# Optimization experiments

Hardware: AMD Instinct MI355X
Metric: run time of the kernel (lower is better)

## Reference

```python
import jax, jax.numpy as jnp
import numpy as np
from jax import lax

B, S, F, H, C = 256, 14, 1024, 1024, 2513


def setup_inputs() -> dict:
    key = jax.random.key(0)
    ks = jax.random.split(key, 12)
    s = 1.0 / np.sqrt(H)  # PyTorch LSTM/Linear init range
    u = lambda k, shape: jax.random.uniform(k, shape, jnp.float32, -s, s)
    return {
        "inputs": jax.random.normal(ks[0], (B, S, F), jnp.float32),
        # rolling LSTM params (PyTorch gate order: i, f, g, o)
        "Wih_r": u(ks[1], (4 * H, F)), "Whh_r": u(ks[2], (4 * H, H)),
        "bih_r": u(ks[3], (4 * H,)), "bhh_r": u(ks[4], (4 * H,)),
        # unrolling LSTM params
        "Wih_u": u(ks[5], (4 * H, F)), "Whh_u": u(ks[6], (4 * H, H)),
        "bih_u": u(ks[7], (4 * H,)), "bhh_u": u(ks[8], (4 * H,)),
        # classifier
        "Wc": u(ks[9], (C, H)), "bc": u(ks[10], (C,)),
    }


def _gate_update(gates, c):
    i, f, g, o = jnp.split(gates, 4, axis=-1)
    c2 = jax.nn.sigmoid(f) * c + jax.nn.sigmoid(i) * jnp.tanh(g)
    h2 = jax.nn.sigmoid(o) * jnp.tanh(c2)
    return h2, c2


def reference(inputs, Wih_r, Whh_r, bih_r, bhh_r, Wih_u, Whh_u, bih_u, bhh_u, Wc, bc):
    # dropout layers are identity (eval mode)
    x = inputs.transpose(1, 0, 2)  # [S, B, F]

    # --- rolling LSTM: collect h, c at every timestep ---
    xg_r = jnp.einsum('sbf,gf->sbg', x, Wih_r) + bih_r + bhh_r  # [S,B,4H]

    def roll_step(carry, xg_t):
        h, c = carry
        h2, c2 = _gate_update(xg_t + h @ Whh_r.T, c)
        return (h2, c2), (h2, c2)

    z = jnp.zeros((B, H), inputs.dtype)
    _, (hs, cs) = lax.scan(roll_step, (z, z), xg_r)  # [S,B,H] each

    # --- unrolling LSTM: for each t, feed inputs[t] repeated (S - t + 1) times,
    # starting from (hs[t], cs[t]); keep the final hidden state.
    # Vectorized: run S+1 steps for every t, gather step index S-t.
    xg_u = jnp.einsum('sbf,gf->sbg', x, Wih_u) + bih_u + bhh_u  # [S,B,4H] (input constant per t)

    def unroll_one(xg_t, h0, c0):
        def step(carry, _):
            h, c = carry
            h2, c2 = _gate_update(xg_t + h @ Whh_u.T, c)
            return (h2, c2), h2
        _, hs_all = lax.scan(step, (h0, c0), None, length=S + 1)
        return hs_all  # [S+1, B, H]

    allh = jax.vmap(unroll_one)(xg_u, hs, cs)  # [S, S+1, B, H]
    t_idx = jnp.arange(S)
    h_n = allh[t_idx, S - t_idx]  # last hidden of each length-(S-t+1) unroll -> [S,B,H]

    preds = h_n.transpose(1, 0, 2)  # [B, S, H]
    y = preds @ Wc.T + bc  # [B, S, C]
    return y
```

## Files before the change

### kernel.cpp

```cpp
#include <hip/hip_runtime.h>
#include <hip/hip_bf16.h>

#define GLOBAL_AS __attribute__((address_space(1)))
#define LDS_AS    __attribute__((address_space(3)))

typedef __bf16 bf16_t;
typedef __bf16 bf16x8 __attribute__((ext_vector_type(8)));
typedef __bf16 bf16x4 __attribute__((ext_vector_type(4)));
typedef float  f32x4  __attribute__((ext_vector_type(4)));
typedef _Float16 fp16_t;
typedef _Float16 fp16x8 __attribute__((ext_vector_type(8)));

static constexpr int Bb = 256;
static constexpr int Ss = 14;
static constexpr int Hh = 1024;
static constexpr int Cc = 2513;
static constexpr int NXc = 3584;
static constexpr int Kk = 1024;

__device__ __forceinline__ float sigm(float x)   { return 1.0f / (1.0f + __expf(-x)); }
__device__ __forceinline__ float tanh_f(float x) { return 2.0f / (1.0f + __expf(-2.0f * x)) - 1.0f; }

template<int EPI>
__global__ __launch_bounds__(256, 2)
void gemm_bt(const bf16_t* __restrict__ A, const bf16_t* __restrict__ Bm,
             int N, int rpg, int cpg, int CG, int CB,
             const float* __restrict__ e_bias,
             bf16_t* __restrict__ xg_bf,
             float* __restrict__ fout)
{
    const int lin = blockIdx.x;
    const int xcd = lin & 7;
    const int per = lin >> 3;
    const int rg = xcd / CG, cg = xcd % CG;
    const int rb = rg * rpg + per % rpg;
    const int cb = cg * cpg + per / rpg;
    if (cb >= CB) return;

    __shared__ char smem[32768];
    LDS_AS char* sA = (LDS_AS char*)smem;
    LDS_AS char* sB = sA + 16384;

    const int tid  = threadIdx.x;
    const int lane = tid & 63;
    const int wave = tid >> 6;
    const int row0 = rb * 128;
    const int col0 = cb * 128;
    const int mwb  = (wave >> 1) * 64;
    const int nwb  = (wave & 1) * 64;
    const int quad = lane >> 4;
    const int l15  = lane & 15;

    f32x4 acc[4][4] = {};

    for (int kb = 0; kb < Kk; kb += 64) {
#pragma unroll
        for (int it = 0; it < 4; ++it) {
            int c  = it * 256 + tid;
            int m  = c >> 3;
            int kq = (c & 7) ^ (m & 7);
            size_t arow;
            if (EPI == 2) {
                int row = row0 + m;
                int bb = row / 14;
                int ss = row - bb * 14;
                arow = (size_t)(ss * 256 + bb);
            } else {
                arow = (size_t)(row0 + m);
            }
            const bf16_t* ga = A + arow * Kk + kb + kq * 8;
            int nr = col0 + m;
            if (EPI == 2) { if (nr >= N) nr = 0; }
            const bf16_t* gb = Bm + (size_t)nr * Kk + kb + kq * 8;
            LDS_AS char* la = sA + (size_t)(it * 256 + (tid & 192)) * 16;
            LDS_AS char* lb = sB + (size_t)(it * 256 + (tid & 192)) * 16;
            __builtin_amdgcn_global_load_lds((const GLOBAL_AS void*)ga, (LDS_AS void*)la, 16, 0, 0);
            __builtin_amdgcn_global_load_lds((const GLOBAL_AS void*)gb, (LDS_AS void*)lb, 16, 0, 0);
        }
        __syncthreads();

#pragma unroll
        for (int kt = 0; kt < 2; ++kt) {
            bf16x8 af[4], bfr[4];
            const int kq = kt * 4 + quad;
#pragma unroll
            for (int i = 0; i < 4; ++i) {
                int ml = mwb + i * 16 + l15;
                af[i]  = *(const LDS_AS bf16x8*)(sA + (size_t)(ml * 8 + (kq ^ (ml & 7))) * 16);
                int nl = nwb + i * 16 + l15;
                bfr[i] = *(const LDS_AS bf16x8*)(sB + (size_t)(nl * 8 + (kq ^ (nl & 7))) * 16);
            }
#pragma unroll
            for (int i = 0; i < 4; ++i)
#pragma unroll
                for (int j = 0; j < 4; ++j)
                    acc[i][j] = __builtin_amdgcn_mfma_f32_16x16x32_bf16(af[i], bfr[j], acc[i][j], 0, 0, 0);
        }
        __syncthreads();
    }

#pragma unroll
    for (int im = 0; im < 4; ++im) {
#pragma unroll
        for (int jn = 0; jn < 4; ++jn) {
            const int rr  = row0 + mwb + im * 16 + quad * 4;
            const int col = col0 + nwb + jn * 16 + l15;
            f32x4 v = acc[im][jn];
            if (EPI == 0) {
                const int n = rr >> 2;
                f32x4 bi = *(const f32x4*)(e_bias + n * 4);
                bf16x4 o;
                o[0] = (bf16_t)(v[0] + bi[0]); o[1] = (bf16_t)(v[1] + bi[1]);
                o[2] = (bf16_t)(v[2] + bi[2]); o[3] = (bf16_t)(v[3] + bi[3]);
                *(bf16x4*)(xg_bf + ((size_t)n * NXc + col) * 4) = o;
            } else {
                if (col < N) {
                    float bi = e_bias[col];
#pragma unroll
                    for (int g = 0; g < 4; ++g)
                        fout[(size_t)(rr + g) * N + col] = v[g] + bi;
                }
            }
        }
    }
}

struct StepArgs {
    const bf16_t* Au;
    const bf16_t* Ar;
    const bf16_t* Bh;
    const bf16_t* xg_u;
    const bf16_t* xg_r;
    const fp16_t* c_r;
    fp16_t*       c_w;
    bf16_t*       h_w;
    const bf16_t* Wih;
    const bf16_t* Xb;
    const float*  bias2;
    bf16_t*       XG2;
    int UCB;
    int b_off;
    int xg_off;
    int cr_off;
    int cw_off;
    int CB, cpg;
    int nRec;
    int xp[7];
};

__global__ __launch_bounds__(256, 2)
void lstm_step(StepArgs p)
{
    const int tid  = threadIdx.x;
    const int lane = tid & 63;
    const int wave = tid >> 6;
    const int mwb  = (wave >> 1) * 64;
    const int nwb  = (wave & 1) * 64;
    const int quad = lane >> 4;
    const int l15  = lane & 15;

    __shared__ char smem[32768];
    LDS_AS char* sA = (LDS_AS char*)smem;
    LDS_AS char* sB = sA + 16384;

    const bf16_t* A;
    const bf16_t* Bbase;
    int row0, bcol0;
    bool isxp;
    bool roll = false;
    int  colb = 0;

    if ((int)blockIdx.x >= p.nRec) {
        isxp = true;
        const int idx = (int)blockIdx.x - p.nRec;
        const int c   = p.xp[idx >> 6];
        const int isu = (c >= 14) ? 1 : 0;
        const int j   = c - isu * 14;
        const int rb  = idx & 31;
        const int cbl = (idx >> 5) & 1;
        row0  = isu * 4096 + rb * 128;
        bcol0 = j * 256 + cbl * 128;
        A     = p.Wih;
        Bbase = p.Xb;
    } else {
        isxp = false;
        const int lin = blockIdx.x;
        const int xcd = lin & 7;
        const int per = lin >> 3;
        const int rb = (xcd >> 2) * 16 + (per & 15);
        const int cb = (xcd & 3) * p.cpg + (per >> 4);
        if (cb >= p.CB) return;
        roll = (cb >= p.UCB);
        colb = roll ? (cb - p.UCB) : cb;
        A     = roll ? p.Ar : p.Au;
        Bbase = p.Bh;
        row0  = rb * 128;
        bcol0 = colb * 128 + (roll ? p.b_off : 0);
    }

    f32x4 acc[4][4] = {};

    for (int kb = 0; kb < Kk; kb += 64) {
#pragma unroll
        for (int it = 0; it < 4; ++it) {
            int c  = it * 256 + tid;
            int m  = c >> 3;
            int kq = (c & 7) ^ (m & 7);
            const bf16_t* ga = A     + (size_t)(row0  + m) * Kk + kb + kq * 8;
            const bf16_t* gb = Bbase + (size_t)(bcol0 + m) * Kk + kb + kq * 8;
            LDS_AS char* la = sA + (size_t)(it * 256 + (tid & 192)) * 16;
            LDS_AS char* lb = sB + (size_t)(it * 256 + (tid & 192)) * 16;
            __builtin_amdgcn_global_load_lds((const GLOBAL_AS void*)ga, (LDS_AS void*)la, 16, 0, 0);
            __builtin_amdgcn_global_load_lds((const GLOBAL_AS void*)gb, (LDS_AS void*)lb, 16, 0, 0);
        }
        __syncthreads();

#pragma unroll
        for (int kt = 0; kt < 2; ++kt) {
            bf16x8 af[4], bfr[4];
            const int kq = kt * 4 + quad;
#pragma unroll
            for (int i = 0; i < 4; ++i) {
                int ml = mwb + i * 16 + l15;
                af[i]  = *(const LDS_AS bf16x8*)(sA + (size_t)(ml * 8 + (kq ^ (ml & 7))) * 16);
                int nl = nwb + i * 16 + l15;
                bfr[i] = *(const LDS_AS bf16x8*)(sB + (size_t)(nl * 8 + (kq ^ (nl & 7))) * 16);
            }
#pragma unroll
            for (int i = 0; i < 4; ++i)
#pragma unroll
                for (int j = 0; j < 4; ++j)
                    acc[i][j] = __builtin_amdgcn_mfma_f32_16x16x32_bf16(af[i], bfr[j], acc[i][j], 0, 0, 0);
        }
        __syncthreads();
    }

    if (isxp) {
#pragma unroll
        for (int im = 0; im < 4; ++im) {
#pragma unroll
            for (int jn = 0; jn < 4; ++jn) {
                const int rr  = row0 + mwb + im * 16 + quad * 4;
                const int col = bcol0 + nwb + jn * 16 + l15;
                f32x4 v = acc[im][jn];
                const int n = rr >> 2;
                f32x4 bi = *(const f32x4*)(p.bias2 + n * 4);
                bf16x4 o;
                o[0] = (bf16_t)(v[0] + bi[0]); o[1] = (bf16_t)(v[1] + bi[1]);
                o[2] = (bf16_t)(v[2] + bi[2]); o[3] = (bf16_t)(v[3] + bi[3]);
                *(bf16x4*)(p.XG2 + ((size_t)n * NXc + col) * 4) = o;
            }
        }
        return;
    }

    const bf16_t* xg = roll ? p.xg_r : p.xg_u;
    const int xo  = roll ? p.xg_off : 0;
    const int cro = roll ? p.cr_off : 0;
    const int cwo = roll ? p.cw_off : 0;
    const int nbase = row0 >> 2;

#pragma unroll
    for (int im = 0; im < 4; ++im)
#pragma unroll
        for (int jn = 0; jn < 4; ++jn) {
            const int rr  = row0 + mwb + im * 16 + quad * 4;
            const int col = colb * 128 + nwb + jn * 16 + l15;
            const int n = rr >> 2;
            bf16x4 xg4 = *(const bf16x4*)(xg + ((size_t)n * NXc + (col + xo)) * 4);
            acc[im][jn][0] += (float)xg4[0];
            acc[im][jn][1] += (float)xg4[1];
            acc[im][jn][2] += (float)xg4[2];
            acc[im][jn][3] += (float)xg4[3];
        }

    LDS_AS f32x4* sG = (LDS_AS f32x4*)smem;

#pragma unroll
    for (int pass = 0; pass < 2; ++pass) {
        if ((wave & 1) == pass) {
            const int nw = (wave >> 1) * 16;
#pragma unroll
            for (int im = 0; im < 4; ++im)
#pragma unroll
                for (int jn = 0; jn < 4; ++jn) {
                    const int n_l = nw + im * 4 + quad;
                    const int c_l = jn * 16 + l15;
                    sG[c_l * 32 + (n_l ^ (c_l & 7))] = acc[im][jn];
                }
        }
        __syncthreads();
        {
            const int c_l  = tid >> 2;
            const int nb   = (tid & 3) * 8;
            const int colg = colb * 128 + pass * 64 + c_l;
            const fp16_t* crp = p.c_r + (size_t)(colg + cro) * Hh + nbase + nb;
            fp16x8 c8 = *(const fp16x8*)crp;
            bf16x8 h8o; fp16x8 c8o;
#pragma unroll
            for (int j = 0; j < 8; ++j) {
                f32x4 g = sG[c_l * 32 + ((nb + j) ^ (c_l & 7))];
                float c2 = sigm(g[1]) * (float)c8[j] + sigm(g[0]) * tanh_f(g[2]);
                float h2 = sigm(g[3]) * tanh_f(c2);
                c8o[j] = (fp16_t)c2;
                h8o[j] = (bf16_t)h2;
            }
            *(fp16x8*)(p.c_w + (size_t)(colg + cwo) * Hh + nbase + nb) = c8o;
            *(bf16x8*)(p.h_w + (size_t)(colg + cwo) * Hh + nbase + nb) = h8o;
        }
        if (pass == 0) __syncthreads();
    }
}

__global__ void cvt_w(const float* __restrict__ a0, const float* __restrict__ a1,
                      const float* __restrict__ a2, const float* __restrict__ a3,
                      bf16_t* __restrict__ o0, bf16_t* __restrict__ o1,
                      bf16_t* __restrict__ o2, bf16_t* __restrict__ o3)
{
    int idx = blockIdx.x * 256 + threadIdx.x;
    int mat = idx >> 20;
    int r   = (idx >> 8) & 4095;
    int k4  = (idx & 255) * 4;
    int n = r >> 2, g = r & 3;
    const float* src = mat == 0 ? a0 : mat == 1 ? a1 : mat == 2 ? a2 : a3;
    bf16_t*      dst = mat == 0 ? o0 : mat == 1 ? o1 : mat == 2 ? o2 : o3;
    f32x4 v = *(const f32x4*)(src + (size_t)(g * Hh + n) * Kk + k4);
    bf16x4 o;
    o[0] = (bf16_t)v[0]; o[1] = (bf16_t)v[1]; o[2] = (bf16_t)v[2]; o[3] = (bf16_t)v[3];
    *(bf16x4*)(dst + (size_t)r * Kk + k4) = o;
}

__global__ void cvt_bias(const float* __restrict__ bih_r, const float* __restrict__ bhh_r,
                         const float* __restrict__ bih_u, const float* __restrict__ bhh_u,
                         float* __restrict__ br, float* __restrict__ bu)
{
    int r = blockIdx.x * 256 + threadIdx.x;
    int n = r >> 2, g = r & 3;
    int ir = g * Hh + n;
    br[r] = bih_r[ir] + bhh_r[ir];
    bu[r] = bih_u[ir] + bhh_u[ir];
}

__global__ void cvt_x(const float* __restrict__ src, bf16_t* __restrict__ dst)
{
    int idx = blockIdx.x * 256 + threadIdx.x;
    int f4  = (idx & 255) * 4;
    int row = idx >> 8;
    int s = row % 14, b = row / 14;
    f32x4 v = *(const f32x4*)(src + (size_t)row * Kk + f4);
    bf16x4 o;
    o[0] = (bf16_t)v[0]; o[1] = (bf16_t)v[1]; o[2] = (bf16_t)v[2]; o[3] = (bf16_t)v[3];
    *(bf16x4*)(dst + (size_t)(s * 256 + b) * Kk + f4) = o;
}

__global__ void cast_f32_bf16(const float* __restrict__ src, bf16_t* __restrict__ dst, int n4)
{
    int i = blockIdx.x * 256 + threadIdx.x;
    if (i < n4) {
        f32x4 v = *(const f32x4*)(src + (size_t)i * 4);
        bf16x4 o;
        o[0] = (bf16_t)v[0]; o[1] = (bf16_t)v[1]; o[2] = (bf16_t)v[2]; o[3] = (bf16_t)v[3];
        *(bf16x4*)(dst + (size_t)i * 4) = o;
    }
}

extern "C" void kernel_launch(void* const* d_in, const int* in_sizes, int n_in,
                              void* d_out, int out_size, void* d_ws, size_t ws_size,
                              hipStream_t stream)
{
    const float* x_in  = (const float*)d_in[0];
    const float* Wih_r = (const float*)d_in[1];
    const float* Whh_r = (const float*)d_in[2];
    const float* bih_r = (const float*)d_in[3];
    const float* bhh_r = (const float*)d_in[4];
    const float* Wih_u = (const float*)d_in[5];
    const float* Whh_u = (const float*)d_in[6];
    const float* bih_u = (const float*)d_in[7];
    const float* bhh_u = (const float*)d_in[8];
    const float* Wc    = (const float*)d_in[9];
    const float* bc    = (const float*)d_in[10];
    float* out = (float*)d_out;

    char* ws = (char*)d_ws;
    size_t off = 0;
    auto alloc = [&](size_t bytes) -> char* {
        char* p = ws + off;
        off += (bytes + 255) & ~(size_t)255;
        return p;
    };

    const size_t BH = (size_t)Bb * Hh;
    bf16_t* w_ih2  = (bf16_t*)alloc((size_t)8192 * Kk * 2);
    bf16_t* w_hhr  = (bf16_t*)alloc((size_t)4096 * Kk * 2);
    bf16_t* w_hhu  = (bf16_t*)alloc((size_t)4096 * Kk * 2);
    bf16_t* wc_b   = (bf16_t*)alloc((size_t)Cc * Kk * 2);
    bf16_t* x_b    = (bf16_t*)alloc((size_t)NXc * Kk * 2);
    float*  bias2  = (float*)alloc(8192 * 4);
    bf16_t* XG2    = (bf16_t*)alloc((size_t)2048 * NXc * 4 * 2);
    bf16_t* P0     = (bf16_t*)alloc((size_t)Ss * BH * 2);
    bf16_t* P1     = (bf16_t*)alloc((size_t)Ss * BH * 2);
    fp16_t* Cp0    = (fp16_t*)alloc((size_t)Ss * BH * 2);
    fp16_t* Cp1    = (fp16_t*)alloc((size_t)Ss * BH * 2);
    bf16_t* h0     = (bf16_t*)alloc(BH * 2);
    fp16_t* c0     = (fp16_t*)alloc(BH * 2);

    bf16_t* XGr = XG2;
    bf16_t* XGu = XG2 + (size_t)1024 * NXc * 4;
    bf16_t* P[2] = {P0, P1};
    fp16_t* Cp[2] = {Cp0, Cp1};

    hipMemsetAsync(h0, 0, BH * 2, stream);
    hipMemsetAsync(c0, 0, BH * 2, stream);

    cvt_w<<<16384, 256, 0, stream>>>(Wih_r, Whh_r, Wih_u, Whh_u,
                                     w_ih2, w_hhr, w_ih2 + (size_t)4096 * Kk, w_hhu);
    cvt_bias<<<16, 256, 0, stream>>>(bih_r, bhh_r, bih_u, bhh_u, bias2, bias2 + 4096);
    cvt_x<<<3584, 256, 0, stream>>>(x_in, x_b);
    cast_f32_bf16<<<(Cc * Kk / 4 + 255) / 256, 256, 0, stream>>>(Wc, wc_b, Cc * Kk / 4);

    static const int xp_sched[6][7] = {
        { 1, 14,  2, 15,  3, 16,  4},
        {17,  5, 18,  6, 19,  7, -1},
        {20,  8, 21,  9, 22, -1, -1},
        {10, 23, 11, 24, -1, -1, -1},
        {12, 25, 13, -1, -1, -1, -1},
        {26, 27, -1, -1, -1, -1, -1},
    };
    static const int xp_n[6] = {7, 6, 5, 4, 3, 2};

    {
        StepArgs p{};
        p.Au = w_hhu; p.Ar = w_hhr; p.Bh = h0;
        p.xg_u = XGu; p.xg_r = XGr;
        p.c_r = c0; p.c_w = Cp[0]; p.h_w = P[0];
        p.Wih = w_ih2; p.Xb = x_b; p.bias2 = bias2; p.XG2 = XG2;
        p.UCB = 0; p.b_off = 0; p.xg_off = 0; p.cr_off = 0; p.cw_off = 0;
        p.CB = 0; p.cpg = 1;
        p.nRec = 0;
        p.xp[0] = 0;
        for (int i = 1; i < 7; ++i) p.xp[i] = -1;
        lstm_step<<<64, 256, 0, stream>>>(p);
    }

    for (int k = 1; k <= 16; ++k) {
        int a = (k - 1 < 14) ? (k - 1) : 14;
        int rollk = (k <= 14) ? 1 : 0;
        StepArgs p{};
        p.Au = w_hhu;  p.Ar = w_hhr;
        p.Bh = (k == 1) ? h0 : P[(k - 1) & 1];
        p.xg_u = XGu;  p.xg_r = XGr;
        p.c_r = (k == 1) ? c0 : Cp[(k - 1) & 1];
        p.c_w = Cp[k & 1];
        p.h_w = P[k & 1];
        p.Wih = w_ih2; p.Xb = x_b; p.bias2 = bias2; p.XG2 = XG2;
        p.UCB = 2 * a;
        p.b_off  = (k >= 2) ? (k - 2) * 256 : 0;
        p.xg_off = (k - 1) * 256;
        p.cr_off = (k >= 2) ? (k - 2) * 256 : 0;
        p.cw_off = (k - 1) * 256;
        p.CB  = p.UCB + 2 * rollk;
        p.cpg = (p.CB + 3) >> 2;
        p.nRec = 8 * 16 * p.cpg;
        int nxp = (k <= 6) ? xp_n[k - 1] : 0;
        for (int i = 0; i < 7; ++i)
            p.xp[i] = (k <= 6 && i < nxp) ? xp_sched[k - 1][i] : -1;
        lstm_step<<<p.nRec + nxp * 64, 256, 0, stream>>>(p);
    }

    gemm_bt<2><<<560, 256, 0, stream>>>(P[0], wc_b, Cc, 14, 5, 4, 20,
                                        bc, nullptr, out);
}
```

Baseline: 748.8 us.

## Double-buffer LDS tiles with async global-to-LDS prefetch in GEMM kernels

Both the generic GEMM and the per-step LSTM kernel now use two 32KB LDS buffers. The next two K-tiles are prefetched with global_load_lds while the current tile is computed, and explicit vmcnt waits replace the full syncthreads after each load. The goal is to hide global memory latency behind the MFMA work. LDS use per block doubles to 64KB, which may limit the intended two blocks per CU, and correctness relies on the hand-written waitcnt counts.

```diff
diff --git a/kernel.cpp b/kernel.cpp
--- a/kernel.cpp
+++ b/kernel.cpp
@@ -37,9 +37,8 @@
     const int cb = cg * cpg + per / rpg;
     if (cb >= CB) return;
 
-    __shared__ char smem[32768];
-    LDS_AS char* sA = (LDS_AS char*)smem;
-    LDS_AS char* sB = sA + 16384;
+    __shared__ char smem[65536];
+    LDS_AS char* sM = (LDS_AS char*)smem;
 
     const int tid  = threadIdx.x;
     const int lane = tid & 63;
@@ -53,7 +52,7 @@
 
     f32x4 acc[4][4] = {};
 
-    for (int kb = 0; kb < Kk; kb += 64) {
+    auto stage = [&](int boff, int kb) {
 #pragma unroll
         for (int it = 0; it < 4; ++it) {
             int c  = it * 256 + tid;
@@ -72,13 +71,13 @@
             int nr = col0 + m;
             if (EPI == 2) { if (nr >= N) nr = 0; }
             const bf16_t* gb = Bm + (size_t)nr * Kk + kb + kq * 8;
-            LDS_AS char* la = sA + (size_t)(it * 256 + (tid & 192)) * 16;
-            LDS_AS char* lb = sB + (size_t)(it * 256 + (tid & 192)) * 16;
+            LDS_AS char* la = sM + boff +         (size_t)(it * 256 + (tid & 192)) * 16;
+            LDS_AS char* lb = sM + boff + 16384 + (size_t)(it * 256 + (tid & 192)) * 16;
             __builtin_amdgcn_global_load_lds((const GLOBAL_AS void*)ga, (LDS_AS void*)la, 16, 0, 0);
             __builtin_amdgcn_global_load_lds((const GLOBAL_AS void*)gb, (LDS_AS void*)lb, 16, 0, 0);
         }
-        __syncthreads();
-
+    };
+    auto compute = [&](int boff) {
 #pragma unroll
         for (int kt = 0; kt < 2; ++kt) {
             bf16x8 af[4], bfr[4];
@@ -86,9 +85,9 @@
 #pragma unroll
             for (int i = 0; i < 4; ++i) {
                 int ml = mwb + i * 16 + l15;
-                af[i]  = *(const LDS_AS bf16x8*)(sA + (size_t)(ml * 8 + (kq ^ (ml & 7))) * 16);
+                af[i]  = *(const LDS_AS bf16x8*)(sM + boff + (size_t)(ml * 8 + (kq ^ (ml & 7))) * 16);
                 int nl = nwb + i * 16 + l15;
-                bfr[i] = *(const LDS_AS bf16x8*)(sB + (size_t)(nl * 8 + (kq ^ (nl & 7))) * 16);
+                bfr[i] = *(const LDS_AS bf16x8*)(sM + boff + 16384 + (size_t)(nl * 8 + (kq ^ (nl & 7))) * 16);
             }
 #pragma unroll
             for (int i = 0; i < 4; ++i)
@@ -96,8 +95,29 @@
                 for (int j = 0; j < 4; ++j)
                     acc[i][j] = __builtin_amdgcn_mfma_f32_16x16x32_bf16(af[i], bfr[j], acc[i][j], 0, 0, 0);
         }
-        __syncthreads();
-    }
+    };
+
+    stage(0, 0);
+    stage(32768, 64);
+    int boff = 0;
+    for (int t = 0; t < 14; ++t) {
+        asm volatile("s_waitcnt vmcnt(8)" ::: "memory");
+        __builtin_amdgcn_s_barrier();
+        compute(boff);
+        asm volatile("s_waitcnt lgkmcnt(0)" ::: "memory");
+        __builtin_amdgcn_sched_barrier(0);
+        __builtin_amdgcn_s_barrier();
+        stage(boff, (t + 2) * 64);
+        boff ^= 32768;
+    }
+    asm volatile("s_waitcnt vmcnt(8)" ::: "memory");
+    __builtin_amdgcn_s_barrier();
+    compute(boff);
+    boff ^= 32768;
+    asm volatile("s_waitcnt vmcnt(0)" ::: "memory");
+    __builtin_amdgcn_s_barrier();
+    compute(boff);
+    __syncthreads();
 
 #pragma unroll
     for (int im = 0; im < 4; ++im) {
@@ -159,9 +179,8 @@
     const int quad = lane >> 4;
     const int l15  = lane & 15;
 
-    __shared__ char smem[32768];
-    LDS_AS char* sA = (LDS_AS char*)smem;
-    LDS_AS char* sB = sA + 16384;
+    __shared__ char smem[65536];
+    LDS_AS char* sM = (LDS_AS char*)smem;
 
     const bf16_t* A;
     const bf16_t* Bbase;
@@ -200,7 +219,7 @@
 
     f32x4 acc[4][4] = {};
 
-    for (int kb = 0; kb < Kk; kb += 64) {
+    auto stage = [&](int boff, int kb) {
 #pragma unroll
         for (int it = 0; it < 4; ++it) {
             int c  = it * 256 + tid;
@@ -208,13 +227,13 @@
             int kq = (c & 7) ^ (m & 7);
             const bf16_t* ga = A     + (size_t)(row0  + m) * Kk + kb + kq * 8;
             const bf16_t* gb = Bbase + (size_t)(bcol0 + m) * Kk + kb + kq * 8;
-            LDS_AS char* la = sA + (size_t)(it * 256 + (tid & 192)) * 16;
-            LDS_AS char* lb = sB + (size_t)(it * 256 + (tid & 192)) * 16;
+            LDS_AS char* la = sM + boff +         (size_t)(it * 256 + (tid & 192)) * 16;
+            LDS_AS char* lb = sM + boff + 16384 + (size_t)(it * 256 + (tid & 192)) * 16;
             __builtin_amdgcn_global_load_lds((const GLOBAL_AS void*)ga, (LDS_AS void*)la, 16, 0, 0);
             __builtin_amdgcn_global_load_lds((const GLOBAL_AS void*)gb, (LDS_AS void*)lb, 16, 0, 0);
         }
-        __syncthreads();
-
+    };
+    auto compute = [&](int boff) {
 #pragma unroll
         for (int kt = 0; kt < 2; ++kt) {
             bf16x8 af[4], bfr[4];
@@ -222,9 +241,9 @@
 #pragma unroll
             for (int i = 0; i < 4; ++i) {
                 int ml = mwb + i * 16 + l15;
-                af[i]  = *(const LDS_AS bf16x8*)(sA + (size_t)(ml * 8 + (kq ^ (ml & 7))) * 16);
+                af[i]  = *(const LDS_AS bf16x8*)(sM + boff + (size_t)(ml * 8 + (kq ^ (ml & 7))) * 16);
                 int nl = nwb + i * 16 + l15;
-                bfr[i] = *(const LDS_AS bf16x8*)(sB + (size_t)(nl * 8 + (kq ^ (nl & 7))) * 16);
+                bfr[i] = *(const LDS_AS bf16x8*)(sM + boff + 16384 + (size_t)(nl * 8 + (kq ^ (nl & 7))) * 16);
             }
 #pragma unroll
             for (int i = 0; i < 4; ++i)
@@ -232,8 +251,29 @@
                 for (int j = 0; j < 4; ++j)
                     acc[i][j] = __builtin_amdgcn_mfma_f32_16x16x32_bf16(af[i], bfr[j], acc[i][j], 0, 0, 0);
         }
-        __syncthreads();
-    }
+    };
+
+    stage(0, 0);
+    stage(32768, 64);
+    int boff = 0;
+    for (int t = 0; t < 14; ++t) {
+        asm volatile("s_waitcnt vmcnt(8)" ::: "memory");
+        __builtin_amdgcn_s_barrier();
+        compute(boff);
+        asm volatile("s_waitcnt lgkmcnt(0)" ::: "memory");
+        __builtin_amdgcn_sched_barrier(0);
+        __builtin_amdgcn_s_barrier();
+        stage(boff, (t + 2) * 64);
+        boff ^= 32768;
+    }
+    asm volatile("s_waitcnt vmcnt(8)" ::: "memory");
+    __builtin_amdgcn_s_barrier();
+    compute(boff);
+    boff ^= 32768;
+    asm volatile("s_waitcnt vmcnt(0)" ::: "memory");
+    __builtin_amdgcn_s_barrier();
+    compute(boff);
+    __syncthreads();
 
     if (isxp) {
 #pragma unroll
```

Result: slower. 772.7 us (+3.2%).

## Widen GEMM and LSTM step tiles to 128x256 and compress input-projection schedule

Applied to the files above, without the earlier changes.

Both the classifier GEMM and the fused LSTM step kernel now compute a 128x256 output tile per block, using two B buffers and two accumulator sets so each A tile loaded into LDS is reused twice. Block counts are halved accordingly, and the input-projection blocks are packed into the first two step launches instead of spreading over six. The aim is less A-operand traffic and fewer blocks per step. In exchange, LDS use rises to 48KB and accumulator registers double, which may hurt occupancy under launch_bounds(256,2). Fewer blocks per recurrent step also means less parallelism across the GPU's compute units.

```diff
diff --git a/kernel.cpp b/kernel.cpp
--- a/kernel.cpp
+++ b/kernel.cpp
@@ -37,21 +37,23 @@
     const int cb = cg * cpg + per / rpg;
     if (cb >= CB) return;
 
-    __shared__ char smem[32768];
-    LDS_AS char* sA = (LDS_AS char*)smem;
-    LDS_AS char* sB = sA + 16384;
+    __shared__ char smem[49152];
+    LDS_AS char* sA  = (LDS_AS char*)smem;
+    LDS_AS char* sB0 = sA + 16384;
+    LDS_AS char* sB1 = sA + 32768;
 
     const int tid  = threadIdx.x;
     const int lane = tid & 63;
     const int wave = tid >> 6;
     const int row0 = rb * 128;
-    const int col0 = cb * 128;
+    const int col0 = cb * 256;
     const int mwb  = (wave >> 1) * 64;
     const int nwb  = (wave & 1) * 64;
     const int quad = lane >> 4;
     const int l15  = lane & 15;
 
-    f32x4 acc[4][4] = {};
+    f32x4 accL[4][4] = {};
+    f32x4 accR[4][4] = {};
 
     for (int kb = 0; kb < Kk; kb += 64) {
 #pragma unroll
@@ -69,56 +71,64 @@
                 arow = (size_t)(row0 + m);
             }
             const bf16_t* ga = A + arow * Kk + kb + kq * 8;
-            int nr = col0 + m;
-            if (EPI == 2) { if (nr >= N) nr = 0; }
-            const bf16_t* gb = Bm + (size_t)nr * Kk + kb + kq * 8;
-            LDS_AS char* la = sA + (size_t)(it * 256 + (tid & 192)) * 16;
-            LDS_AS char* lb = sB + (size_t)(it * 256 + (tid & 192)) * 16;
-            __builtin_amdgcn_global_load_lds((const GLOBAL_AS void*)ga, (LDS_AS void*)la, 16, 0, 0);
-            __builtin_amdgcn_global_load_lds((const GLOBAL_AS void*)gb, (LDS_AS void*)lb, 16, 0, 0);
+            int nr0 = col0 + m;
+            int nr1 = col0 + 128 + m;
+            if (EPI == 2) { if (nr0 >= N) nr0 = 0; if (nr1 >= N) nr1 = 0; }
+            const bf16_t* gb0 = Bm + (size_t)nr0 * Kk + kb + kq * 8;
+            const bf16_t* gb1 = Bm + (size_t)nr1 * Kk + kb + kq * 8;
+            const size_t lofs = (size_t)(it * 256 + (tid & 192)) * 16;
+            __builtin_amdgcn_global_load_lds((const GLOBAL_AS void*)ga,  (LDS_AS void*)(sA  + lofs), 16, 0, 0);
+            __builtin_amdgcn_global_load_lds((const GLOBAL_AS void*)gb0, (LDS_AS void*)(sB0 + lofs), 16, 0, 0);
+            __builtin_amdgcn_global_load_lds((const GLOBAL_AS void*)gb1, (LDS_AS void*)(sB1 + lofs), 16, 0, 0);
         }
         __syncthreads();
 
 #pragma unroll
         for (int kt = 0; kt < 2; ++kt) {
-            bf16x8 af[4], bfr[4];
+            bf16x8 af[4], bfL[4], bfR[4];
             const int kq = kt * 4 + quad;
 #pragma unroll
             for (int i = 0; i < 4; ++i) {
                 int ml = mwb + i * 16 + l15;
-                af[i]  = *(const LDS_AS bf16x8*)(sA + (size_t)(ml * 8 + (kq ^ (ml & 7))) * 16);
+                af[i]  = *(const LDS_AS bf16x8*)(sA  + (size_t)(ml * 8 + (kq ^ (ml & 7))) * 16);
                 int nl = nwb + i * 16 + l15;
-                bfr[i] = *(const LDS_AS bf16x8*)(sB + (size_t)(nl * 8 + (kq ^ (nl & 7))) * 16);
+                bfL[i] = *(const LDS_AS bf16x8*)(sB0 + (size_t)(nl * 8 + (kq ^ (nl & 7))) * 16);
+                bfR[i] = *(const LDS_AS bf16x8*)(sB1 + (size_t)(nl * 8 + (kq ^ (nl & 7))) * 16);
             }
 #pragma unroll
             for (int i = 0; i < 4; ++i)
 #pragma unroll
-                for (int j = 0; j < 4; ++j)
-                    acc[i][j] = __builtin_amdgcn_mfma_f32_16x16x32_bf16(af[i], bfr[j], acc[i][j], 0, 0, 0);
+                for (int j = 0; j < 4; ++j) {
+                    accL[i][j] = __builtin_amdgcn_mfma_f32_16x16x32_bf16(af[i], bfL[j], accL[i][j], 0, 0, 0);
+                    accR[i][j] = __builtin_amdgcn_mfma_f32_16x16x32_bf16(af[i], bfR[j], accR[i][j], 0, 0, 0);
+                }
         }
         __syncthreads();
     }
 
 #pragma unroll
-    for (int im = 0; im < 4; ++im) {
-#pragma unroll
-        for (int jn = 0; jn < 4; ++jn) {
-            const int rr  = row0 + mwb + im * 16 + quad * 4;
-            const int col = col0 + nwb + jn * 16 + l15;
-            f32x4 v = acc[im][jn];
-            if (EPI == 0) {
-                const int n = rr >> 2;
-                f32x4 bi = *(const f32x4*)(e_bias + n * 4);
-                bf16x4 o;
-                o[0] = (bf16_t)(v[0] + bi[0]); o[1] = (bf16_t)(v[1] + bi[1]);
-                o[2] = (bf16_t)(v[2] + bi[2]); o[3] = (bf16_t)(v[3] + bi[3]);
-                *(bf16x4*)(xg_bf + ((size_t)n * NXc + col) * 4) = o;
-            } else {
-                if (col < N) {
-                    float bi = e_bias[col];
-#pragma unroll
-                    for (int g = 0; g < 4; ++g)
-                        fout[(size_t)(rr + g) * N + col] = v[g] + bi;
+    for (int half = 0; half < 2; ++half) {
+#pragma unroll
+        for (int im = 0; im < 4; ++im) {
+#pragma unroll
+            for (int jn = 0; jn < 4; ++jn) {
+                const int rr  = row0 + mwb + im * 16 + quad * 4;
+                const int col = col0 + half * 128 + nwb + jn * 16 + l15;
+                f32x4 v = half ? accR[im][jn] : accL[im][jn];
+                if (EPI == 0) {
+                    const int n = rr >> 2;
+                    f32x4 bi = *(const f32x4*)(e_bias + n * 4);
+                    bf16x4 o;
+                    o[0] = (bf16_t)(v[0] + bi[0]); o[1] = (bf16_t)(v[1] + bi[1]);
+                    o[2] = (bf16_t)(v[2] + bi[2]); o[3] = (bf16_t)(v[3] + bi[3]);
+                    *(bf16x4*)(xg_bf + ((size_t)n * NXc + col) * 4) = o;
+                } else {
+                    if (col < N) {
+                        float bi = e_bias[col];
+#pragma unroll
+                        for (int g = 0; g < 4; ++g)
+                            fout[(size_t)(rr + g) * N + col] = v[g] + bi;
+                    }
                 }
             }
         }
@@ -138,14 +148,14 @@
     const bf16_t* Xb;
     const float*  bias2;
     bf16_t*       XG2;
-    int UCB;
+    int UCP;
     int b_off;
     int xg_off;
     int cr_off;
     int cw_off;
-    int CB, cpg;
+    int CP, cppg;
     int nRec;
-    int xp[7];
+    int xp[15];
 };
 
 __global__ __launch_bounds__(256, 2)
@@ -159,27 +169,27 @@
     const int quad = lane >> 4;
     const int l15  = lane & 15;
 
-    __shared__ char smem[32768];
-    LDS_AS char* sA = (LDS_AS char*)smem;
-    LDS_AS char* sB = sA + 16384;
+    __shared__ char smem[49152];
+    LDS_AS char* sA  = (LDS_AS char*)smem;
+    LDS_AS char* sB0 = sA + 16384;
+    LDS_AS char* sB1 = sA + 32768;
 
     const bf16_t* A;
     const bf16_t* Bbase;
     int row0, bcol0;
     bool isxp;
     bool roll = false;
-    int  colb = 0;
+    int  colp = 0;
 
     if ((int)blockIdx.x >= p.nRec) {
         isxp = true;
         const int idx = (int)blockIdx.x - p.nRec;
-        const int c   = p.xp[idx >> 6];
+        const int c   = p.xp[idx >> 5];
         const int isu = (c >= 14) ? 1 : 0;
         const int j   = c - isu * 14;
         const int rb  = idx & 31;
-        const int cbl = (idx >> 5) & 1;
         row0  = isu * 4096 + rb * 128;
-        bcol0 = j * 256 + cbl * 128;
+        bcol0 = j * 256;
         A     = p.Wih;
         Bbase = p.Xb;
     } else {
@@ -188,17 +198,18 @@
         const int xcd = lin & 7;
         const int per = lin >> 3;
         const int rb = (xcd >> 2) * 16 + (per & 15);
-        const int cb = (xcd & 3) * p.cpg + (per >> 4);
-        if (cb >= p.CB) return;
-        roll = (cb >= p.UCB);
-        colb = roll ? (cb - p.UCB) : cb;
+        const int cp = (xcd & 3) * p.cppg + (per >> 4);
+        if (cp >= p.CP) return;
+        roll = (cp >= p.UCP);
+        colp = roll ? (cp - p.UCP) : cp;
         A     = roll ? p.Ar : p.Au;
         Bbase = p.Bh;
         row0  = rb * 128;
-        bcol0 = colb * 128 + (roll ? p.b_off : 0);
-    }
-
-    f32x4 acc[4][4] = {};
+        bcol0 = colp * 256 + (roll ? p.b_off : 0);
+    }
+
+    f32x4 accL[4][4] = {};
+    f32x4 accR[4][4] = {};
 
     for (int kb = 0; kb < Kk; kb += 64) {
 #pragma unroll
@@ -206,49 +217,56 @@
             int c  = it * 256 + tid;
             int m  = c >> 3;
             int kq = (c & 7) ^ (m & 7);
-            const bf16_t* ga = A     + (size_t)(row0  + m) * Kk + kb + kq * 8;
-            const bf16_t* gb = Bbase + (size_t)(bcol0 + m) * Kk + kb + kq * 8;
-            LDS_AS char* la = sA + (size_t)(it * 256 + (tid & 192)) * 16;
-            LDS_AS char* lb = sB + (size_t)(it * 256 + (tid & 192)) * 16;
-            __builtin_amdgcn_global_load_lds((const GLOBAL_AS void*)ga, (LDS_AS void*)la, 16, 0, 0);
-            __builtin_amdgcn_global_load_lds((const GLOBAL_AS void*)gb, (LDS_AS void*)lb, 16, 0, 0);
+            const bf16_t* ga  = A     + (size_t)(row0  + m) * Kk + kb + kq * 8;
+            const bf16_t* gb0 = Bbase + (size_t)(bcol0 + m) * Kk + kb + kq * 8;
+            const bf16_t* gb1 = Bbase + (size_t)(bcol0 + 128 + m) * Kk + kb + kq * 8;
+            const size_t lofs = (size_t)(it * 256 + (tid & 192)) * 16;
+            __builtin_amdgcn_global_load_lds((const GLOBAL_AS void*)ga,  (LDS_AS void*)(sA  + lofs), 16, 0, 0);
+            __builtin_amdgcn_global_load_lds((const GLOBAL_AS void*)gb0, (LDS_AS void*)(sB0 + lofs), 16, 0, 0);
+            __builtin_amdgcn_global_load_lds((const GLOBAL_AS void*)gb1, (LDS_AS void*)(sB1 + lofs), 16, 0, 0);
         }
         __syncthreads();
 
 #pragma unroll
         for (int kt = 0; kt < 2; ++kt) {
-            bf16x8 af[4], bfr[4];
+            bf16x8 af[4], bfL[4], bfR[4];
             const int kq = kt * 4 + quad;
 #pragma unroll
             for (int i = 0; i < 4; ++i) {
                 int ml = mwb + i * 16 + l15;
-                af[i]  = *(const LDS_AS bf16x8*)(sA + (size_t)(ml * 8 + (kq ^ (ml & 7))) * 16);
+                af[i]  = *(const LDS_AS bf16x8*)(sA  + (size_t)(ml * 8 + (kq ^ (ml & 7))) * 16);
                 int nl = nwb + i * 16 + l15;
-                bfr[i] = *(const LDS_AS bf16x8*)(sB + (size_t)(nl * 8 + (kq ^ (nl & 7))) * 16);
+                bfL[i] = *(const LDS_AS bf16x8*)(sB0 + (size_t)(nl * 8 + (kq ^ (nl & 7))) * 16);
+                bfR[i] = *(const LDS_AS bf16x8*)(sB1 + (size_t)(nl * 8 + (kq ^ (nl & 7))) * 16);
             }
 #pragma unroll
             for (int i = 0; i < 4; ++i)
 #pragma unroll
-                for (int j = 0; j < 4; ++j)
-                    acc[i][j] = __builtin_amdgcn_mfma_f32_16x16x32_bf16(af[i], bfr[j], acc[i][j], 0, 0, 0);
+                for (int j = 0; j < 4; ++j) {
+                    accL[i][j] = __builtin_amdgcn_mfma_f32_16x16x32_bf16(af[i], bfL[j], accL[i][j], 0, 0, 0);
+                    accR[i][j] = __builtin_amdgcn_mfma_f32_16x16x32_bf16(af[i], bfR[j], accR[i][j], 0, 0, 0);
+                }
         }
         __syncthreads();
     }
 
     if (isxp) {
 #pragma unroll
-        for (int im = 0; im < 4; ++im) {
-#pragma unroll
-            for (int jn = 0; jn < 4; ++jn) {
-                const int rr  = row0 + mwb + im * 16 + quad * 4;
-                const int col = bcol0 + nwb + jn * 16 + l15;
-                f32x4 v = acc[im][jn];
-                const int n = rr >> 2;
-                f32x4 bi = *(const f32x4*)(p.bias2 + n * 4);
-                bf16x4 o;
-                o[0] = (bf16_t)(v[0] + bi[0]); o[1] = (bf16_t)(v[1] + bi[1]);
-                o[2] = (bf16_t)(v[2] + bi[2]); o[3] = (bf16_t)(v[3] + bi[3]);
-                *(bf16x4*)(p.XG2 + ((size_t)n * NXc + col) * 4) = o;
+        for (int half = 0; half < 2; ++half) {
+#pragma unroll
+            for (int im = 0; im < 4; ++im) {
+#pragma unroll
+                for (int jn = 0; jn < 4; ++jn) {
+                    const int rr  = row0 + mwb + im * 16 + quad * 4;
+                    const int col = bcol0 + half * 128 + nwb + jn * 16 + l15;
+                    f32x4 v = half ? accR[im][jn] : accL[im][jn];
+                    const int n = rr >> 2;
+                    f32x4 bi = *(const f32x4*)(p.bias2 + n * 4);
+                    bf16x4 o;
+                    o[0] = (bf16_t)(v[0] + bi[0]); o[1] = (bf16_t)(v[1] + bi[1]);
+                    o[2] = (bf16_t)(v[2] + bi[2]); o[3] = (bf16_t)(v[3] + bi[3]);
+                    *(bf16x4*)(p.XG2 + ((size_t)n * NXc + col) * 4) = o;
+                }
             }
         }
         return;
@@ -259,57 +277,59 @@
     const int cro = roll ? p.cr_off : 0;
     const int cwo = roll ? p.cw_off : 0;
     const int nbase = row0 >> 2;
-
-#pragma unroll
-    for (int im = 0; im < 4; ++im)
-#pragma unroll
-        for (int jn = 0; jn < 4; ++jn) {
-            const int rr  = row0 + mwb + im * 16 + quad * 4;
-            const int col = colb * 128 + nwb + jn * 16 + l15;
-            const int n = rr >> 2;
-            bf16x4 xg4 = *(const bf16x4*)(xg + ((size_t)n * NXc + (col + xo)) * 4);
-            acc[im][jn][0] += (float)xg4[0];
-            acc[im][jn][1] += (float)xg4[1];
-            acc[im][jn][2] += (float)xg4[2];
-            acc[im][jn][3] += (float)xg4[3];
-        }
-
     LDS_AS f32x4* sG = (LDS_AS f32x4*)smem;
 
-#pragma unroll
-    for (int pass = 0; pass < 2; ++pass) {
-        if ((wave & 1) == pass) {
-            const int nw = (wave >> 1) * 16;
-#pragma unroll
-            for (int im = 0; im < 4; ++im)
-#pragma unroll
-                for (int jn = 0; jn < 4; ++jn) {
-                    const int n_l = nw + im * 4 + quad;
-                    const int c_l = jn * 16 + l15;
-                    sG[c_l * 32 + (n_l ^ (c_l & 7))] = acc[im][jn];
+    auto epi = [&](f32x4 (&acc)[4][4], int colbase) {
+#pragma unroll
+        for (int im = 0; im < 4; ++im)
+#pragma unroll
+            for (int jn = 0; jn < 4; ++jn) {
+                const int rr  = row0 + mwb + im * 16 + quad * 4;
+                const int col = colbase + nwb + jn * 16 + l15;
+                const int n = rr >> 2;
+                bf16x4 xg4 = *(const bf16x4*)(xg + ((size_t)n * NXc + (col + xo)) * 4);
+                acc[im][jn][0] += (float)xg4[0];
+                acc[im][jn][1] += (float)xg4[1];
+                acc[im][jn][2] += (float)xg4[2];
+                acc[im][jn][3] += (float)xg4[3];
+            }
+#pragma unroll
+        for (int pass = 0; pass < 2; ++pass) {
+            if ((wave & 1) == pass) {
+                const int nw = (wave >> 1) * 16;
+#pragma unroll
+                for (int im = 0; im < 4; ++im)
+#pragma unroll
+                    for (int jn = 0; jn < 4; ++jn) {
+                        const int n_l = nw + im * 4 + quad;
+                        const int c_l = jn * 16 + l15;
+                        sG[c_l * 32 + (n_l ^ (c_l & 7))] = acc[im][jn];
+                    }
+            }
+            __syncthreads();
+            {
+                const int c_l  = tid >> 2;
+                const int nb   = (tid & 3) * 8;
+                const int colg = colbase + pass * 64 + c_l;
+                const fp16_t* crp = p.c_r + (size_t)(colg + cro) * Hh + nbase + nb;
+                fp16x8 c8 = *(const fp16x8*)crp;
+                bf16x8 h8o; fp16x8 c8o;
+#pragma unroll
+                for (int j = 0; j < 8; ++j) {
+                    f32x4 g = sG[c_l * 32 + ((nb + j) ^ (c_l & 7))];
+                    float c2 = sigm(g[1]) * (float)c8[j] + sigm(g[0]) * tanh_f(g[2]);
+                    float h2 = sigm(g[3]) * tanh_f(c2);
+                    c8o[j] = (fp16_t)c2;
+                    h8o[j] = (bf16_t)h2;
                 }
-        }
-        __syncthreads();
-        {
-            const int c_l  = tid >> 2;
-            const int nb   = (tid & 3) * 8;
-            const int colg = colb * 128 + pass * 64 + c_l;
-            const fp16_t* crp = p.c_r + (size_t)(colg + cro) * Hh + nbase + nb;
-            fp16x8 c8 = *(const fp16x8*)crp;
-            bf16x8 h8o; fp16x8 c8o;
-#pragma unroll
-            for (int j = 0; j < 8; ++j) {
-                f32x4 g = sG[c_l * 32 + ((nb + j) ^ (c_l & 7))];
-                float c2 = sigm(g[1]) * (float)c8[j] + sigm(g[0]) * tanh_f(g[2]);
-                float h2 = sigm(g[3]) * tanh_f(c2);
-                c8o[j] = (fp16_t)c2;
-                h8o[j] = (bf16_t)h2;
-            }
-            *(fp16x8*)(p.c_w + (size_t)(colg + cwo) * Hh + nbase + nb) = c8o;
-            *(bf16x8*)(p.h_w + (size_t)(colg + cwo) * Hh + nbase + nb) = h8o;
-        }
-        if (pass == 0) __syncthreads();
-    }
+                *(fp16x8*)(p.c_w + (size_t)(colg + cwo) * Hh + nbase + nb) = c8o;
+                *(bf16x8*)(p.h_w + (size_t)(colg + cwo) * Hh + nbase + nb) = h8o;
+            }
+            __syncthreads();
+        }
+    };
+    epi(accL, colp * 256);
+    epi(accR, colp * 256 + 128);
 }
 
 __global__ void cvt_w(const float* __restrict__ a0, const float* __restrict__ a1,
@@ -418,15 +438,11 @@
     cvt_x<<<3584, 256, 0, stream>>>(x_in, x_b);
     cast_f32_bf16<<<(Cc * Kk / 4 + 255) / 256, 256, 0, stream>>>(Wc, wc_b, Cc * Kk / 4);
 
-    static const int xp_sched[6][7] = {
-        { 1, 14,  2, 15,  3, 16,  4},
-        {17,  5, 18,  6, 19,  7, -1},
-        {20,  8, 21,  9, 22, -1, -1},
-        {10, 23, 11, 24, -1, -1, -1},
-        {12, 25, 13, -1, -1, -1, -1},
-        {26, 27, -1, -1, -1, -1, -1},
+    static const int xp_sched[2][15] = {
+        { 1, 14,  2, 15,  3, 16,  4, 17,  5, 18,  6, 19,  7, 20,  8},
+        {21,  9, 22, 10, 23, 11, 24, 12, 25, 13, 26, 27, -1, -1, -1},
     };
-    static const int xp_n[6] = {7, 6, 5, 4, 3, 2};
+    static const int xp_n[2] = {15, 12};
 
     {
         StepArgs p{};
@@ -434,12 +450,12 @@
         p.xg_u = XGu; p.xg_r = XGr;
         p.c_r = c0; p.c_w = Cp[0]; p.h_w = P[0];
         p.Wih = w_ih2; p.Xb = x_b; p.bias2 = bias2; p.XG2 = XG2;
-        p.UCB = 0; p.b_off = 0; p.xg_off = 0; p.cr_off = 0; p.cw_off = 0;
-        p.CB = 0; p.cpg = 1;
+        p.UCP = 0; p.b_off = 0; p.xg_off = 0; p.cr_off = 0; p.cw_off = 0;
+        p.CP = 0; p.cppg = 1;
         p.nRec = 0;
         p.xp[0] = 0;
-        for (int i = 1; i < 7; ++i) p.xp[i] = -1;
-        lstm_step<<<64, 256, 0, stream>>>(p);
+        for (int i = 1; i < 15; ++i) p.xp[i] = -1;
+        lstm_step<<<32, 256, 0, stream>>>(p);
     }
 
     for (int k = 1; k <= 16; ++k) {
@@ -453,20 +469,20 @@
         p.c_w = Cp[k & 1];
         p.h_w = P[k & 1];
         p.Wih = w_ih2; p.Xb = x_b; p.bias2 = bias2; p.XG2 = XG2;
-        p.UCB = 2 * a;
+        p.UCP = a;
         p.b_off  = (k >= 2) ? (k - 2) * 256 : 0;
         p.xg_off = (k - 1) * 256;
         p.cr_off = (k >= 2) ? (k - 2) * 256 : 0;
         p.cw_off = (k - 1) * 256;
-        p.CB  = p.UCB + 2 * rollk;
-        p.cpg = (p.CB + 3) >> 2;
-        p.nRec = 8 * 16 * p.cpg;
-        int nxp = (k <= 6) ? xp_n[k - 1] : 0;
-        for (int i = 0; i < 7; ++i)
-            p.xp[i] = (k <= 6 && i < nxp) ? xp_sched[k - 1][i] : -1;
-        lstm_step<<<p.nRec + nxp * 64, 256, 0, stream>>>(p);
-    }
-
-    gemm_bt<2><<<560, 256, 0, stream>>>(P[0], wc_b, Cc, 14, 5, 4, 20,
+        p.CP   = a + rollk;
+        p.cppg = (p.CP + 3) >> 2;
+        p.nRec = 8 * 16 * p.cppg;
+        int nxp = (k <= 2) ? xp_n[k - 1] : 0;
+        for (int i = 0; i < 15; ++i)
+            p.xp[i] = (k <= 2 && i < nxp) ? xp_sched[k - 1][i] : -1;
+        lstm_step<<<p.nRec + nxp * 32, 256, 0, stream>>>(p);
+    }
+
+    gemm_bt<2><<<336, 256, 0, stream>>>(P[0], wc_b, Cc, 14, 3, 4, 10,
                                         bc, nullptr, out);
 }
```

New measurement: 839.5 us. +12.1%, slower.

## Use 2-wave 128-thread blocks with wider per-wave tiles and compress input-projection schedule

Applied to the files above, without the earlier changes.

The LSTM step kernel moves from 4 waves of 64x64 sub-tiles to 2 waves that each compute a 64x128 sub-tile, doubling accumulators per thread and reusing more B fragments from LDS. The gate epilogue is reworked so both waves write their gates and each thread handles two chunks. The input-projection tiles that were spread over the first six recurrent steps are packed into the first two steps. This is meant to improve MFMA-to-LDS-read ratio and cut per-block overhead, at the cost of higher register pressure and a heavier load on the first two steps.

```diff
diff --git a/kernel.cpp b/kernel.cpp
--- a/kernel.cpp
+++ b/kernel.cpp
@@ -145,17 +145,15 @@
     int cw_off;
     int CB, cpg;
     int nRec;
-    int xp[7];
+    int xp[14];
 };
 
-__global__ __launch_bounds__(256, 2)
+__global__ __launch_bounds__(128, 2)
 void lstm_step(StepArgs p)
 {
     const int tid  = threadIdx.x;
     const int lane = tid & 63;
     const int wave = tid >> 6;
-    const int mwb  = (wave >> 1) * 64;
-    const int nwb  = (wave & 1) * 64;
     const int quad = lane >> 4;
     const int l15  = lane & 15;
 
@@ -198,18 +196,18 @@
         bcol0 = colb * 128 + (roll ? p.b_off : 0);
     }
 
-    f32x4 acc[4][4] = {};
+    f32x4 acc[4][8] = {};
 
     for (int kb = 0; kb < Kk; kb += 64) {
 #pragma unroll
-        for (int it = 0; it < 4; ++it) {
-            int c  = it * 256 + tid;
+        for (int it = 0; it < 8; ++it) {
+            int c  = it * 128 + tid;
             int m  = c >> 3;
             int kq = (c & 7) ^ (m & 7);
             const bf16_t* ga = A     + (size_t)(row0  + m) * Kk + kb + kq * 8;
             const bf16_t* gb = Bbase + (size_t)(bcol0 + m) * Kk + kb + kq * 8;
-            LDS_AS char* la = sA + (size_t)(it * 256 + (tid & 192)) * 16;
-            LDS_AS char* lb = sB + (size_t)(it * 256 + (tid & 192)) * 16;
+            LDS_AS char* la = sA + (size_t)(it * 128 + (tid & 64)) * 16;
+            LDS_AS char* lb = sB + (size_t)(it * 128 + (tid & 64)) * 16;
             __builtin_amdgcn_global_load_lds((const GLOBAL_AS void*)ga, (LDS_AS void*)la, 16, 0, 0);
             __builtin_amdgcn_global_load_lds((const GLOBAL_AS void*)gb, (LDS_AS void*)lb, 16, 0, 0);
         }
@@ -217,19 +215,22 @@
 
 #pragma unroll
         for (int kt = 0; kt < 2; ++kt) {
-            bf16x8 af[4], bfr[4];
+            bf16x8 af[4], bfr[8];
             const int kq = kt * 4 + quad;
 #pragma unroll
             for (int i = 0; i < 4; ++i) {
-                int ml = mwb + i * 16 + l15;
+                int ml = wave * 64 + i * 16 + l15;
                 af[i]  = *(const LDS_AS bf16x8*)(sA + (size_t)(ml * 8 + (kq ^ (ml & 7))) * 16);
-                int nl = nwb + i * 16 + l15;
-                bfr[i] = *(const LDS_AS bf16x8*)(sB + (size_t)(nl * 8 + (kq ^ (nl & 7))) * 16);
+            }
+#pragma unroll
+            for (int j = 0; j < 8; ++j) {
+                int nl = j * 16 + l15;
+                bfr[j] = *(const LDS_AS bf16x8*)(sB + (size_t)(nl * 8 + (kq ^ (nl & 7))) * 16);
             }
 #pragma unroll
             for (int i = 0; i < 4; ++i)
 #pragma unroll
-                for (int j = 0; j < 4; ++j)
+                for (int j = 0; j < 8; ++j)
                     acc[i][j] = __builtin_amdgcn_mfma_f32_16x16x32_bf16(af[i], bfr[j], acc[i][j], 0, 0, 0);
         }
         __syncthreads();
@@ -239,9 +240,9 @@
 #pragma unroll
         for (int im = 0; im < 4; ++im) {
 #pragma unroll
-            for (int jn = 0; jn < 4; ++jn) {
-                const int rr  = row0 + mwb + im * 16 + quad * 4;
-                const int col = bcol0 + nwb + jn * 16 + l15;
+            for (int jn = 0; jn < 8; ++jn) {
+                const int rr  = row0 + wave * 64 + im * 16 + quad * 4;
+                const int col = bcol0 + jn * 16 + l15;
                 f32x4 v = acc[im][jn];
                 const int n = rr >> 2;
                 f32x4 bi = *(const f32x4*)(p.bias2 + n * 4);
@@ -263,9 +264,9 @@
 #pragma unroll
     for (int im = 0; im < 4; ++im)
 #pragma unroll
-        for (int jn = 0; jn < 4; ++jn) {
-            const int rr  = row0 + mwb + im * 16 + quad * 4;
-            const int col = colb * 128 + nwb + jn * 16 + l15;
+        for (int jn = 0; jn < 8; ++jn) {
+            const int rr  = row0 + wave * 64 + im * 16 + quad * 4;
+            const int col = colb * 128 + jn * 16 + l15;
             const int n = rr >> 2;
             bf16x4 xg4 = *(const bf16x4*)(xg + ((size_t)n * NXc + (col + xo)) * 4);
             acc[im][jn][0] += (float)xg4[0];
@@ -278,21 +279,20 @@
 
 #pragma unroll
     for (int pass = 0; pass < 2; ++pass) {
-        if ((wave & 1) == pass) {
-            const int nw = (wave >> 1) * 16;
-#pragma unroll
-            for (int im = 0; im < 4; ++im)
-#pragma unroll
-                for (int jn = 0; jn < 4; ++jn) {
-                    const int n_l = nw + im * 4 + quad;
-                    const int c_l = jn * 16 + l15;
-                    sG[c_l * 32 + (n_l ^ (c_l & 7))] = acc[im][jn];
-                }
-        }
+#pragma unroll
+        for (int im = 0; im < 4; ++im)
+#pragma unroll
+            for (int jj = 0; jj < 4; ++jj) {
+                const int jn  = pass * 4 + jj;
+                const int n_l = wave * 16 + im * 4 + quad;
+                const int c_l = jj * 16 + l15;
+                sG[c_l * 32 + (n_l ^ (c_l & 7))] = acc[im][jn];
+            }
         __syncthreads();
-        {
-            const int c_l  = tid >> 2;
-            const int nb   = (tid & 3) * 8;
+#pragma unroll
+        for (int rep = 0; rep < 2; ++rep) {
+            const int c_l  = tid >> 1;
+            const int nb   = (tid & 1) * 8 + rep * 16;
             const int colg = colb * 128 + pass * 64 + c_l;
             const fp16_t* crp = p.c_r + (size_t)(colg + cro) * Hh + nbase + nb;
             fp16x8 c8 = *(const fp16x8*)crp;
@@ -418,15 +418,11 @@
     cvt_x<<<3584, 256, 0, stream>>>(x_in, x_b);
     cast_f32_bf16<<<(Cc * Kk / 4 + 255) / 256, 256, 0, stream>>>(Wc, wc_b, Cc * Kk / 4);
 
-    static const int xp_sched[6][7] = {
-        { 1, 14,  2, 15,  3, 16,  4},
-        {17,  5, 18,  6, 19,  7, -1},
-        {20,  8, 21,  9, 22, -1, -1},
-        {10, 23, 11, 24, -1, -1, -1},
-        {12, 25, 13, -1, -1, -1, -1},
-        {26, 27, -1, -1, -1, -1, -1},
+    static const int xp_sched[2][14] = {
+        { 1, 14,  2, 15,  3, 16,  4, 17,  5, 18,  6, 19,  7, 20},
+        { 8, 21,  9, 22, 10, 23, 11, 24, 12, 25, 13, 26, 27, -1},
     };
-    static const int xp_n[6] = {7, 6, 5, 4, 3, 2};
+    static const int xp_n[2] = {14, 13};
 
     {
         StepArgs p{};
@@ -438,8 +434,8 @@
         p.CB = 0; p.cpg = 1;
         p.nRec = 0;
         p.xp[0] = 0;
-        for (int i = 1; i < 7; ++i) p.xp[i] = -1;
-        lstm_step<<<64, 256, 0, stream>>>(p);
+        for (int i = 1; i < 14; ++i) p.xp[i] = -1;
+        lstm_step<<<64, 128, 0, stream>>>(p);
     }
 
     for (int k = 1; k <= 16; ++k) {
@@ -461,10 +457,10 @@
         p.CB  = p.UCB + 2 * rollk;
         p.cpg = (p.CB + 3) >> 2;
         p.nRec = 8 * 16 * p.cpg;
-        int nxp = (k <= 6) ? xp_n[k - 1] : 0;
-        for (int i = 0; i < 7; ++i)
-            p.xp[i] = (k <= 6 && i < nxp) ? xp_sched[k - 1][i] : -1;
-        lstm_step<<<p.nRec + nxp * 64, 256, 0, stream>>>(p);
+        int nxp = (k <= 2) ? xp_n[k - 1] : 0;
+        for (int i = 0; i < 14; ++i)
+            p.xp[i] = (k <= 2 && i < nxp) ? xp_sched[k - 1][i] : -1;
+        lstm_step<<<p.nRec + nxp * 64, 128, 0, stream>>>(p);
     }
 
     gemm_bt<2><<<560, 256, 0, stream>>>(P[0], wc_b, Cc, 14, 5, 4, 20,
```

Measured after the change: 815.7 us. +8.9%, slower.
